# Performance work log

Measured on AMD Instinct MI355X. Metric: run time of the kernel, lower is better.

The kernel has to match this reference:

```python
import jax, jax.numpy as jnp
import numpy as np
import math

S, B, H, NH = 2048, 1, 4096, 32
D = H // NH  # 128 head dim


def rotate_half(x):
    x1, x2 = x[..., : x.shape[-1] // 2], x[..., x.shape[-1] // 2 :]
    return jnp.concatenate((-x2, x1), axis=-1)


def setup_inputs() -> dict:
    key = jax.random.key(0)
    k1, k2, k3, k4, k5 = jax.random.split(key, 5)
    hidden_states = jax.random.normal(k1, (S, B, H), dtype=jnp.float32)
    position_ids = jnp.broadcast_to(jnp.arange(S, dtype=jnp.int32)[None, :], (B, S))
    # causal mask: True = masked (upper triangle above diagonal)
    attention_mask = jnp.triu(jnp.ones((S, S), dtype=bool), k=1)[None, None]
    W_qkv = jax.random.normal(k2, (H, 3 * H), dtype=jnp.float32) * 0.02
    b_qkv = jax.random.normal(k3, (3 * H,), dtype=jnp.float32) * 0.02
    W_dense = jax.random.normal(k4, (H, H), dtype=jnp.float32) * 0.02
    b_dense = jax.random.normal(k5, (H,), dtype=jnp.float32) * 0.02
    return {
        "hidden_states": hidden_states,
        "position_ids": position_ids,
        "attention_mask": attention_mask,
        "W_qkv": W_qkv,
        "b_qkv": b_qkv,
        "W_dense": W_dense,
        "b_dense": b_dense,
        "layer_id": 27,
    }


def reference(hidden_states, position_ids, attention_mask, W_qkv, b_qkv, W_dense, b_dense, layer_id):
    s, b, h = hidden_states.shape
    nh, d = NH, D
    # QKV projection: [s, b, 3h] -> [s, b, nh, 3d] -> split
    mixed = hidden_states @ W_qkv + b_qkv
    mixed = mixed.reshape(s, b, nh, 3 * d)
    q, k, v = jnp.split(mixed, 3, axis=-1)  # each [s, b, nh, d]
    # rotary embedding indexed by position_ids (transposed to [s, b])
    pos = position_ids.T  # [s, b]
    inv_freq = 1.0 / (10000.0 ** (jnp.arange(0, d, 2, dtype=jnp.float32) / d))
    freqs = pos[..., None].astype(jnp.float32) * inv_freq  # [s, b, d/2]
    emb = jnp.concatenate((freqs, freqs), axis=-1)  # [s, b, d]
    cos = jnp.cos(emb)[:, :, None, :]  # [s, b, 1, d]
    sin = jnp.sin(emb)[:, :, None, :]
    q = q * cos + rotate_half(q) * sin
    k = k * cos + rotate_half(k) * sin
    # attention with per-layer scaling coeff (cancels in softmax except mask fill)
    coeff = jnp.float32(layer_id + 1)
    q_scaled = q / (math.sqrt(d) * coeff)
    scores = jnp.einsum("sbnd,tbnd->bnst", q_scaled, k)  # [b, nh, s, s]
    scores = jnp.where(attention_mask, jnp.float32(-10000.0), scores) * coeff
    probs = jax.nn.softmax(scores, axis=-1)
    ctx = jnp.einsum("bnst,tbnd->sbnd", probs, v).reshape(s, b, h)
    out = ctx @ W_dense + b_dense
    return out
```

## Files before the change

### kernel.cpp

```cpp
#include <hip/hip_runtime.h>

#define S_LEN 2048
#define HID   4096
#define NHEAD 32
#define DHEAD 128
#define H3    12288

typedef __attribute__((ext_vector_type(8))) __bf16 bf16x8;
typedef __attribute__((ext_vector_type(4))) __bf16 bf16x4;
typedef __attribute__((ext_vector_type(4))) float  f32x4;
typedef __attribute__((ext_vector_type(16))) float f32x16;

__device__ __forceinline__ void gl_lds16(const void* g, void* l) {
  __builtin_amdgcn_global_load_lds(
      (const __attribute__((address_space(1))) void*)g,
      (__attribute__((address_space(3))) void*)l, 16, 0, 0);
}

__global__ void cvt_f32_bf16(const float* __restrict__ in, __bf16* __restrict__ out, int n4) {
  int i = blockIdx.x * blockDim.x + threadIdx.x;
  if (i >= n4) return;
  float4 v = ((const float4*)in)[i];
  bf16x4 o;
  o.x = (__bf16)v.x; o.y = (__bf16)v.y; o.z = (__bf16)v.z; o.w = (__bf16)v.w;
  ((bf16x4*)out)[i] = o;
}

__global__ void transpose_cvt(const float* __restrict__ in, __bf16* __restrict__ out, int R, int C) {
  __shared__ float t[64][65];
  const int tid = threadIdx.x;
  const int r0 = blockIdx.y * 64, c0 = blockIdx.x * 64;
#pragma unroll
  for (int p = 0; p < 4; ++p) {
    int r = p * 16 + (tid >> 4);
    int c4 = (tid & 15) * 4;
    float4 v = *(const float4*)(in + (size_t)(r0 + r) * C + c0 + c4);
    t[r][c4] = v.x; t[r][c4 + 1] = v.y; t[r][c4 + 2] = v.z; t[r][c4 + 3] = v.w;
  }
  __syncthreads();
#pragma unroll
  for (int p = 0; p < 4; ++p) {
    int c = p * 16 + (tid >> 4);
    int rg = (tid & 15) * 4;
    bf16x4 o;
    o.x = (__bf16)t[rg][c]; o.y = (__bf16)t[rg + 1][c];
    o.z = (__bf16)t[rg + 2][c]; o.w = (__bf16)t[rg + 3][c];
    *(bf16x4*)(out + (size_t)(c0 + c) * R + r0 + rg) = o;
  }
}

__global__ void rope_kernel(__bf16* __restrict__ q, __bf16* __restrict__ k,
                            const int* __restrict__ pos) {
  int idx = blockIdx.x * 256 + threadIdx.x;
  int j = idx & 63;
  int hs = idx >> 6;
  int s = hs & (S_LEN - 1);
  float p = (float)pos[s];
  float invf = __expf(-(float)j * (9.210340371976184f / 64.f));
  float a = p * invf;
  float c, sn;
  __sincosf(a, &sn, &c);
  const float SC = 0.08838834764831845f;
  size_t base = (size_t)hs * 128;
  float x1 = (float)q[base + j], x2 = (float)q[base + j + 64];
  q[base + j]      = (__bf16)((x1 * c - x2 * sn) * SC);
  q[base + j + 64] = (__bf16)((x2 * c + x1 * sn) * SC);
  x1 = (float)k[base + j]; x2 = (float)k[base + j + 64];
  k[base + j]      = (__bf16)(x1 * c - x2 * sn);
  k[base + j + 64] = (__bf16)(x2 * c + x1 * sn);
}

template <int EPI>
__global__ __launch_bounds__(256, 2)
void gemm_bf16(const __bf16* __restrict__ A, const __bf16* __restrict__ BT,
               const float* __restrict__ bias, int K,
               float* __restrict__ outf) {
  const int tid = threadIdx.x;
  const int lane = tid & 63;
  const int wave = tid >> 6;
  const int bm = blockIdx.x * 128;
  const int bn = blockIdx.y * 128;

  __shared__ __bf16 As[128 * 64];
  __shared__ __bf16 Bs[128 * 64];
  char* Ab = (char*)As;
  char* Bb = (char*)Bs;

  f32x4 acc[4][4] = {};

  const int wm = (wave >> 1) * 64;
  const int wn = (wave & 1) * 64;

  const int sr = tid >> 3;
  const int sc = (tid & 7) * 16;
  const int scs = sc ^ ((sr & 7) << 4);

  const char* Arow = (const char*)(A + (size_t)(bm + sr) * K) + scs;
  const char* Brow = (const char*)(BT + (size_t)(bn + sr) * K) + scs;

  for (int k0 = 0; k0 < K; k0 += 64) {
    const char* a_src = Arow + (size_t)k0 * 2;
    const char* b_src = Brow + (size_t)k0 * 2;
    char* a_dst = Ab + wave * 1024;
    char* b_dst = Bb + wave * 1024;
#pragma unroll
    for (int i = 0; i < 4; ++i) {
      gl_lds16(a_src + (size_t)i * 32 * K * 2, a_dst + i * 4096);
      gl_lds16(b_src + (size_t)i * 32 * K * 2, b_dst + i * 4096);
    }
    __syncthreads();
#pragma unroll
    for (int kk = 0; kk < 2; ++kk) {
      bf16x8 af[4], bfr[4];
#pragma unroll
      for (int m = 0; m < 4; ++m) {
        int row = wm + m * 16 + (lane & 15);
        int cb = (kk * 64 + ((lane >> 4) << 4)) ^ ((row & 7) << 4);
        af[m] = *(const bf16x8*)(Ab + row * 128 + cb);
      }
#pragma unroll
      for (int n = 0; n < 4; ++n) {
        int row = wn + n * 16 + (lane & 15);
        int cb = (kk * 64 + ((lane >> 4) << 4)) ^ ((row & 7) << 4);
        bfr[n] = *(const bf16x8*)(Bb + row * 128 + cb);
      }
#pragma unroll
      for (int m = 0; m < 4; ++m)
#pragma unroll
        for (int n = 0; n < 4; ++n)
          acc[m][n] = __builtin_amdgcn_mfma_f32_16x16x32_bf16(af[m], bfr[n], acc[m][n], 0, 0, 0);
    }
    __syncthreads();
  }

  const int rbase = (lane >> 4) << 2;
  const int cl = lane & 15;
#pragma unroll
  for (int n = 0; n < 4; ++n) {
    const int col = bn + wn + n * 16 + cl;
    const float bv = bias[col];
#pragma unroll
    for (int m = 0; m < 4; ++m) {
      const int srow = bm + wm + m * 16 + rbase;
#pragma unroll
      for (int r = 0; r < 4; ++r)
        outf[(size_t)(srow + r) * HID + col] = acc[m][n][r] + bv;
    }
  }
}

template <int EPI>
__global__ __launch_bounds__(256, 2)
void gemm32(const __bf16* __restrict__ A, const __bf16* __restrict__ BT,
            const float* __restrict__ bias, int K,
            __bf16* __restrict__ outq, __bf16* __restrict__ outk,
            __bf16* __restrict__ outvt) {
  const int tid = threadIdx.x;
  const int lane = tid & 63;
  const int wave = tid >> 6;
  const int bm = blockIdx.x * 256;
  const int bn = blockIdx.y * 128;

  __shared__ char lds[49152];
  char* Ab = lds;
  char* Bb = lds + 32768;

  f32x16 acc[4][2] = {};

  const int wm = (wave >> 1) * 128;
  const int wn = (wave & 1) * 64;
  const int l31 = lane & 31;
  const int hi = lane >> 5;

  const int sr = tid >> 3;
  const int scb = ((tid & 7) * 16) ^ ((sr & 7) << 4);
  const int K2 = K * 2;
  const char* Arow = (const char*)A + (size_t)(bm + sr) * K2 + scb;
  const char* Brow = (const char*)BT + (size_t)(bn + sr) * K2 + scb;

  for (int k0 = 0; k0 < K; k0 += 64) {
    const char* a_src = Arow + (size_t)k0 * 2;
    const char* b_src = Brow + (size_t)k0 * 2;
    char* a_dst = Ab + wave * 1024;
    char* b_dst = Bb + wave * 1024;
#pragma unroll
    for (int i = 0; i < 8; ++i)
      gl_lds16(a_src + (size_t)i * 32 * K2, a_dst + i * 4096);
#pragma unroll
    for (int i = 0; i < 4; ++i)
      gl_lds16(b_src + (size_t)i * 32 * K2, b_dst + i * 4096);
    __syncthreads();
#pragma unroll
    for (int kk = 0; kk < 4; ++kk) {
      const int cbase = kk * 32 + (hi << 4);
      bf16x8 af[4], bfr[2];
#pragma unroll
      for (int m = 0; m < 4; ++m) {
        const int row = wm + m * 32 + l31;
        af[m] = *(const bf16x8*)(Ab + row * 128 + (cbase ^ ((row & 7) << 4)));
      }
#pragma unroll
      for (int n = 0; n < 2; ++n) {
        const int row = wn + n * 32 + l31;
        bfr[n] = *(const bf16x8*)(Bb + row * 128 + (cbase ^ ((row & 7) << 4)));
      }
#pragma unroll
      for (int m = 0; m < 4; ++m)
#pragma unroll
        for (int n = 0; n < 2; ++n)
          acc[m][n] = __builtin_amdgcn_mfma_f32_32x32x16_bf16(af[m], bfr[n], acc[m][n], 0, 0, 0);
    }
    __syncthreads();
  }

  const int route = (bn >> 7) % 3;
  const int head = bn / 384;
#pragma unroll
  for (int n = 0; n < 2; ++n) {
    const int d = wn + n * 32 + l31;
    const float bv = bias[bn + d];
#pragma unroll
    for (int m = 0; m < 4; ++m) {
      if (route == 2) {
#pragma unroll
        for (int qd = 0; qd < 4; ++qd) {
          const int srow = bm + wm + m * 32 + qd * 8 + (hi << 2);
          bf16x4 o;
          o.x = (__bf16)(acc[m][n][qd * 4 + 0] + bv);
          o.y = (__bf16)(acc[m][n][qd * 4 + 1] + bv);
          o.z = (__bf16)(acc[m][n][qd * 4 + 2] + bv);
          o.w = (__bf16)(acc[m][n][qd * 4 + 3] + bv);
          *(bf16x4*)(outvt + ((size_t)head * 128 + d) * S_LEN + srow) = o;
        }
      } else {
        __bf16* dst = (route == 0 ? outq : outk) + (size_t)head * S_LEN * 128;
#pragma unroll
        for (int r = 0; r < 16; ++r) {
          const int srow = bm + wm + m * 32 + (r & 3) + 8 * (r >> 2) + (hi << 2);
          dst[(size_t)srow * 128 + d] = (__bf16)(acc[m][n][r] + bv);
        }
      }
    }
  }
}

__global__ __launch_bounds__(256, 2)
void attn_kernel(const __bf16* __restrict__ q, const __bf16* __restrict__ k,
                 const __bf16* __restrict__ vt, __bf16* __restrict__ ctx) {
  const int p = blockIdx.x, h = blockIdx.y;
  const int tid = threadIdx.x, lane = tid & 63, wave = tid >> 6;
  __shared__ __bf16 Ks[64 * 128];
  __shared__ __bf16 Vs[128 * 64];
  __shared__ __bf16 Ps[4][16 * 64];
  char* Kb = (char*)Ks;
  char* Vb = (char*)Vs;
  char* Pb = (char*)(Ps[wave]);

  const __bf16* qh = q + (size_t)h * S_LEN * 128;
  const __bf16* kh = k + (size_t)h * S_LEN * 128;
  const __bf16* vh = vt + (size_t)h * 128 * S_LEN;

  const int cl = lane & 15, rbase = (lane >> 4) << 2;

  const int krow = tid >> 4, kcol = (tid & 15) * 16;
  const int kcs = kcol ^ ((krow & 7) << 4);
  const int vrow = tid >> 3, vcol = (tid & 7) * 16;
  const int vcs = vcol ^ ((vrow & 7) << 4);

  for (int half = 0; half < 2; ++half) {
    const int qt = half ? (31 - p) : p;
    const int qrow0 = qt * 64 + wave * 16;

    bf16x8 qf[4];
#pragma unroll
    for (int kk = 0; kk < 4; ++kk)
      qf[kk] = *(const bf16x8*)(qh + (size_t)(qrow0 + cl) * 128 + kk * 32 + ((lane >> 4) << 3));

    f32x4 oacc[8] = {};
    float mrow[4], lrow[4];
#pragma unroll
    for (int r = 0; r < 4; ++r) { mrow[r] = -1e30f; lrow[r] = 0.f; }

    for (int j = 0; j <= qt; ++j) {
      {
        const char* src = (const char*)(kh + (size_t)(j * 64 + krow) * 128) + kcs;
        char* dst = Kb + wave * 1024;
#pragma unroll
        for (int i = 0; i < 4; ++i)
          gl_lds16(src + (size_t)i * 16 * 256, dst + i * 4096);
      }
      {
        const char* src = (const char*)(vh + (size_t)vrow * S_LEN + j * 64) + vcs;
        char* dst = Vb + wave * 1024;
#pragma unroll
        for (int i = 0; i < 4; ++i)
          gl_lds16(src + (size_t)i * 32 * (S_LEN * 2), dst + i * 4096);
      }
      __syncthreads();

      f32x4 sacc[4] = {};
#pragma unroll
      for (int kk = 0; kk < 4; ++kk) {
        bf16x8 bk[4];
#pragma unroll
        for (int n = 0; n < 4; ++n) {
          int row = n * 16 + cl;
          int cb = (kk * 64 + ((lane >> 4) << 4)) ^ ((row & 7) << 4);
          bk[n] = *(const bf16x8*)(Kb + row * 256 + cb);
        }
#pragma unroll
        for (int n = 0; n < 4; ++n)
          sacc[n] = __builtin_amdgcn_mfma_f32_16x16x32_bf16(qf[kk], bk[n], sacc[n], 0, 0, 0);
      }

      float pmax[4];
#pragma unroll
      for (int r = 0; r < 4; ++r) pmax[r] = -1e30f;
      if (j == qt) {
#pragma unroll
        for (int n = 0; n < 4; ++n) {
          const int col = n * 16 + cl;
#pragma unroll
          for (int r = 0; r < 4; ++r) {
            const int row = wave * 16 + rbase + r;
            float sv = (col > row) ? -1e30f : sacc[n][r];
            sacc[n][r] = sv;
            pmax[r] = fmaxf(pmax[r], sv);
          }
        }
      } else {
#pragma unroll
        for (int n = 0; n < 4; ++n)
#pragma unroll
          for (int r = 0; r < 4; ++r)
            pmax[r] = fmaxf(pmax[r], sacc[n][r]);
      }
#pragma unroll
      for (int xm = 1; xm < 16; xm <<= 1)
#pragma unroll
        for (int r = 0; r < 4; ++r)
          pmax[r] = fmaxf(pmax[r], __shfl_xor(pmax[r], xm, 64));

      const bool okd = (pmax[0] <= mrow[0] + 8.f) && (pmax[1] <= mrow[1] + 8.f) &&
                       (pmax[2] <= mrow[2] + 8.f) && (pmax[3] <= mrow[3] + 8.f);
      if (__all(okd)) {
#pragma unroll
        for (int r = 0; r < 4; ++r) {
          float psum = 0.f;
#pragma unroll
          for (int n = 0; n < 4; ++n) {
            float pe = __expf(sacc[n][r] - mrow[r]);
            sacc[n][r] = pe;
            psum += pe;
          }
#pragma unroll
          for (int xm = 1; xm < 16; xm <<= 1)
            psum += __shfl_xor(psum, xm, 64);
          lrow[r] += psum;
        }
      } else {
#pragma unroll
        for (int r = 0; r < 4; ++r) {
          const float mnew = fmaxf(mrow[r], pmax[r]);
          const float alpha = __expf(mrow[r] - mnew);
          mrow[r] = mnew;
          float psum = 0.f;
#pragma unroll
          for (int n = 0; n < 4; ++n) {
            float pe = __expf(sacc[n][r] - mnew);
            sacc[n][r] = pe;
            psum += pe;
          }
#pragma unroll
          for (int xm = 1; xm < 16; xm <<= 1)
            psum += __shfl_xor(psum, xm, 64);
          lrow[r] = lrow[r] * alpha + psum;
#pragma unroll
          for (int nd = 0; nd < 8; ++nd)
            oacc[nd][r] *= alpha;
        }
      }

#pragma unroll
      for (int n = 0; n < 4; ++n) {
        const int colb = (n * 16 + cl) * 2;
#pragma unroll
        for (int r = 0; r < 4; ++r) {
          const int row = rbase + r;
          *(__bf16*)(Pb + row * 128 + (colb ^ ((row & 7) << 4))) = (__bf16)sacc[n][r];
        }
      }

#pragma unroll
      for (int kk = 0; kk < 2; ++kk) {
        bf16x8 pa, bv[8];
        {
          int row = cl;
          int cb = (kk * 64 + ((lane >> 4) << 4)) ^ ((row & 7) << 4);
          pa = *(const bf16x8*)(Pb + row * 128 + cb);
        }
#pragma unroll
        for (int nd = 0; nd < 8; ++nd) {
          int row = nd * 16 + cl;
          int cb = (kk * 64 + ((lane >> 4) << 4)) ^ ((row & 7) << 4);
          bv[nd] = *(const bf16x8*)(Vb + row * 128 + cb);
        }
#pragma unroll
        for (int nd = 0; nd < 8; ++nd)
          oacc[nd] = __builtin_amdgcn_mfma_f32_16x16x32_bf16(pa, bv[nd], oacc[nd], 0, 0, 0);
      }
      __syncthreads();
    }

#pragma unroll
    for (int nd = 0; nd < 8; ++nd) {
      const int d = nd * 16 + cl;
#pragma unroll
      for (int r = 0; r < 4; ++r) {
        const int srow = qrow0 + rbase + r;
        ctx[(size_t)srow * HID + h * 128 + d] = (__bf16)(oacc[nd][r] / lrow[r]);
      }
    }
  }
}

extern "C" void kernel_launch(void* const* d_in, const int* in_sizes, int n_in,
                              void* d_out, int out_size, void* d_ws, size_t ws_size,
                              hipStream_t stream) {
  const float* hs = (const float*)d_in[0];
  const int* pos = (const int*)d_in[1];
  const float* wqkv = (const float*)d_in[3];
  const float* bqkv = (const float*)d_in[4];
  const float* wd = (const float*)d_in[5];
  const float* bd = (const float*)d_in[6];
  float* out = (float*)d_out;

  char* ws = (char*)d_ws;
  const size_t MB = 1024ull * 1024ull;
  if (ws_size < 160 * MB) return;
  __bf16* wT  = (__bf16*)(ws);
  __bf16* xb  = (__bf16*)(ws + 96 * MB);
  __bf16* qb_ = (__bf16*)(ws + 112 * MB);
  __bf16* kb_ = (__bf16*)(ws + 128 * MB);
  __bf16* vtb = (__bf16*)(ws + 144 * MB);

  cvt_f32_bf16<<<8192, 256, 0, stream>>>(hs, xb, 2097152);
  transpose_cvt<<<dim3(192, 64), 256, 0, stream>>>(wqkv, wT, 4096, 12288);
  gemm32<0><<<dim3(8, 96), 256, 0, stream>>>(xb, wT, bqkv, 4096, qb_, kb_, vtb);
  rope_kernel<<<16384, 256, 0, stream>>>(qb_, kb_, pos);
  transpose_cvt<<<dim3(64, 64), 256, 0, stream>>>(wd, wT, 4096, 4096);
  attn_kernel<<<dim3(16, 32), 256, 0, stream>>>(qb_, kb_, vtb, xb);
  gemm_bf16<1><<<dim3(16, 32), 256, 0, stream>>>(xb, wT, bd, 4096, out);
}
```

Measured before the change: 473.0 us.

## Double-buffer LDS tiles in dense GEMM and attention K/V loads

Converts the dense output GEMM and the attention kernel to double-buffered LDS, issuing the async global-to-LDS loads for the next K-tile or K/V tile before computing on the current one. This is meant to hide global memory latency behind MFMA work instead of stalling on a load before every tile. It doubles LDS use per block, to 64KB in the GEMM and about 72KB in attention, which may reduce occupancy. The synchronisation placement relative to buffer reuse is not fully visible and may need care.

```diff
diff --git a/kernel.cpp b/kernel.cpp
--- a/kernel.cpp
+++ b/kernel.cpp
@@ -70,21 +70,17 @@
   k[base + j + 64] = (__bf16)(x2 * c + x1 * sn);
 }
 
-template <int EPI>
 __global__ __launch_bounds__(256, 2)
-void gemm_bf16(const __bf16* __restrict__ A, const __bf16* __restrict__ BT,
-               const float* __restrict__ bias, int K,
-               float* __restrict__ outf) {
+void gemm_dense(const __bf16* __restrict__ A, const __bf16* __restrict__ BT,
+                const float* __restrict__ bias, int K,
+                float* __restrict__ outf) {
   const int tid = threadIdx.x;
   const int lane = tid & 63;
   const int wave = tid >> 6;
   const int bm = blockIdx.x * 128;
   const int bn = blockIdx.y * 128;
 
-  __shared__ __bf16 As[128 * 64];
-  __shared__ __bf16 Bs[128 * 64];
-  char* Ab = (char*)As;
-  char* Bb = (char*)Bs;
+  __shared__ char lds[2][32768];
 
   f32x4 acc[4][4] = {};
 
@@ -98,17 +94,26 @@
   const char* Arow = (const char*)(A + (size_t)(bm + sr) * K) + scs;
   const char* Brow = (const char*)(BT + (size_t)(bn + sr) * K) + scs;
 
-  for (int k0 = 0; k0 < K; k0 += 64) {
-    const char* a_src = Arow + (size_t)k0 * 2;
-    const char* b_src = Brow + (size_t)k0 * 2;
-    char* a_dst = Ab + wave * 1024;
-    char* b_dst = Bb + wave * 1024;
+  const int NT = K >> 6;
+
+  auto stage = [&](int t) {
+    const char* a_src = Arow + (size_t)t * 128;
+    const char* b_src = Brow + (size_t)t * 128;
+    char* a_dst = lds[t & 1] + wave * 1024;
+    char* b_dst = lds[t & 1] + 16384 + wave * 1024;
 #pragma unroll
     for (int i = 0; i < 4; ++i) {
       gl_lds16(a_src + (size_t)i * 32 * K * 2, a_dst + i * 4096);
       gl_lds16(b_src + (size_t)i * 32 * K * 2, b_dst + i * 4096);
     }
-    __syncthreads();
+  };
+
+  stage(0);
+  __syncthreads();
+  for (int t = 0; t < NT; ++t) {
+    if (t + 1 < NT) stage(t + 1);
+    const char* Ab = lds[t & 1];
+    const char* Bb = lds[t & 1] + 16384;
 #pragma unroll
     for (int kk = 0; kk < 2; ++kk) {
       bf16x8 af[4], bfr[4];
@@ -249,11 +254,9 @@
                  const __bf16* __restrict__ vt, __bf16* __restrict__ ctx) {
   const int p = blockIdx.x, h = blockIdx.y;
   const int tid = threadIdx.x, lane = tid & 63, wave = tid >> 6;
-  __shared__ __bf16 Ks[64 * 128];
-  __shared__ __bf16 Vs[128 * 64];
+  __shared__ char Kd[2][16384];
+  __shared__ char Vd[2][16384];
   __shared__ __bf16 Ps[4][16 * 64];
-  char* Kb = (char*)Ks;
-  char* Vb = (char*)Vs;
   char* Pb = (char*)(Ps[wave]);
 
   const __bf16* qh = q + (size_t)h * S_LEN * 128;
@@ -267,6 +270,23 @@
   const int vrow = tid >> 3, vcol = (tid & 7) * 16;
   const int vcs = vcol ^ ((vrow & 7) << 4);
 
+  auto stage_kv = [&](int j) {
+    {
+      const char* src = (const char*)(kh + (size_t)(j * 64 + krow) * 128) + kcs;
+      char* dst = Kd[j & 1] + wave * 1024;
+#pragma unroll
+      for (int i = 0; i < 4; ++i)
+        gl_lds16(src + (size_t)i * 16 * 256, dst + i * 4096);
+    }
+    {
+      const char* src = (const char*)(vh + (size_t)vrow * S_LEN + j * 64) + vcs;
+      char* dst = Vd[j & 1] + wave * 1024;
+#pragma unroll
+      for (int i = 0; i < 4; ++i)
+        gl_lds16(src + (size_t)i * 32 * (S_LEN * 2), dst + i * 4096);
+    }
+  };
+
   for (int half = 0; half < 2; ++half) {
     const int qt = half ? (31 - p) : p;
     const int qrow0 = qt * 64 + wave * 16;
@@ -281,22 +301,14 @@
 #pragma unroll
     for (int r = 0; r < 4; ++r) { mrow[r] = -1e30f; lrow[r] = 0.f; }
 
-    for (int j = 0; j <= qt; ++j) {
-      {
-        const char* src = (const char*)(kh + (size_t)(j * 64 + krow) * 128) + kcs;
-        char* dst = Kb + wave * 1024;
-#pragma unroll
-        for (int i = 0; i < 4; ++i)
-          gl_lds16(src + (size_t)i * 16 * 256, dst + i * 4096);
-      }
-      {
-        const char* src = (const char*)(vh + (size_t)vrow * S_LEN + j * 64) + vcs;
-        char* dst = Vb + wave * 1024;
-#pragma unroll
-        for (int i = 0; i < 4; ++i)
-          gl_lds16(src + (size_t)i * 32 * (S_LEN * 2), dst + i * 4096);
-      }
-      __syncthreads();
+    const int nt = qt + 1;
+    stage_kv(0);
+    __syncthreads();
+
+    for (int j = 0; j < nt; ++j) {
+      if (j + 1 < nt) stage_kv(j + 1);
+      const char* Kb = Kd[j & 1];
+      const char* Vb = Vd[j & 1];
 
       f32x4 sacc[4] = {};
 #pragma unroll
@@ -450,5 +462,5 @@
   rope_kernel<<<16384, 256, 0, stream>>>(qb_, kb_, pos);
   transpose_cvt<<<dim3(64, 64), 256, 0, stream>>>(wd, wT, 4096, 4096);
   attn_kernel<<<dim3(16, 32), 256, 0, stream>>>(qb_, kb_, vtb, xb);
-  gemm_bf16<1><<<dim3(16, 32), 256, 0, stream>>>(xb, wT, bd, 4096, out);
-}
+  gemm_dense<<<dim3(16, 32), 256, 0, stream>>>(xb, wT, bd, 4096, out);
+}
```

New measurement: 461.2 us. 1.03x faster.
